# Kernel tuning notes

Measured on AMD Instinct MI355X. Metric: run time of the kernel, lower is better.

## Reference

```python
import jax, jax.numpy as jnp
import numpy as np
import math

NUM_CLASSES = 80
MAX_ANCHOR_MATCHES = 10
ALPHA = 0.5
BETA = 6.0
EPSILON = 1e-9        # label-encoder epsilon
KEPS = 1e-7           # keras.backend.epsilon() used inside compute_ciou
B, NB = 16, 64        # batch, padded max GT boxes


def make_anchor_points():
    # YOLOv8 @ 640x640: strides 8/16/32 -> 80^2 + 40^2 + 20^2 = 8400 anchors
    pts = []
    for stride, n in [(8, 80), (16, 40), (32, 20)]:
        xs = (jnp.arange(n, dtype=jnp.float32) + 0.5) * stride
        gy, gx = jnp.meshgrid(xs, xs, indexing='ij')
        pts.append(jnp.stack([gx.reshape(-1), gy.reshape(-1)], axis=-1))
    return jnp.concatenate(pts, axis=0)  # (8400, 2)


def setup_inputs() -> dict:
    key = jax.random.key(0)
    k0, k1, k2, k3, k4, k5 = jax.random.split(key, 6)
    anc_points = make_anchor_points()
    NA = anc_points.shape[0]
    pd_scores = jax.random.uniform(k0, (B, NA, NUM_CLASSES), dtype=jnp.float32)
    # predicted boxes roughly centered on anchors
    wh = jax.random.uniform(k1, (B, NA, 2), minval=8.0, maxval=96.0)
    ctr = anc_points[None] + jax.random.normal(k2, (B, NA, 2)) * 8.0
    pd_bboxes = jnp.concatenate([ctr - wh / 2, ctr + wh / 2], axis=-1)
    # ground-truth boxes (xyxy) inside a 640x640 image
    g_wh = jax.random.uniform(k3, (B, NB, 2), minval=16.0, maxval=200.0)
    g_ctr = jax.random.uniform(k4, (B, NB, 2), minval=40.0, maxval=600.0)
    gt_bboxes = jnp.concatenate([g_ctr - g_wh / 2, g_ctr + g_wh / 2], axis=-1)
    gt_labels = jax.random.randint(k5, (B, NB), 0, NUM_CLASSES).astype(jnp.float32)
    # first 48 of 64 padded slots are real boxes
    mask_gt = jnp.broadcast_to(jnp.arange(NB)[None, :, None] < 48, (B, NB, 1))
    return {
        'pd_scores': pd_scores,
        'pd_bboxes': pd_bboxes,
        'anc_points': anc_points,
        'gt_labels': gt_labels,
        'gt_bboxes': gt_bboxes,
        'mask_gt': mask_gt,
    }


def compute_ciou(b1, b2):
    """CIoU between xyxy boxes b1 (gt) and b2 (pred); broadcasts, returns (...,)."""
    x1a, y1a, x2a, y2a = b1[..., 0], b1[..., 1], b1[..., 2], b1[..., 3]
    x1b, y1b, x2b, y2b = b2[..., 0], b2[..., 1], b2[..., 2], b2[..., 3]
    w1 = x2a - x1a
    h1 = y2a - y1a + KEPS
    w2 = x2b - x1b
    h2 = y2b - y1b + KEPS
    inter = (jnp.maximum(jnp.minimum(x2a, x2b) - jnp.maximum(x1a, x1b), 0.0)
             * jnp.maximum(jnp.minimum(y2a, y2b) - jnp.maximum(y1a, y1b), 0.0))
    union = w1 * h1 + w2 * h2 - inter + KEPS
    iou = inter / union
    cw = jnp.maximum(x2a, x2b) - jnp.minimum(x1a, x1b)
    ch = jnp.maximum(y2a, y2b) - jnp.minimum(y1a, y1b)
    c2 = cw * cw + ch * ch + KEPS
    rho2 = ((x1a + x2a) / 2 - (x1b + x2b) / 2) ** 2 + ((y1a + y2a) / 2 - (y1b + y2b) / 2) ** 2
    v = (4.0 / math.pi ** 2) * (jnp.arctan(w2 / h2) - jnp.arctan(w1 / h1)) ** 2
    alpha = v / (v - iou + (1.0 + KEPS))
    return iou - (rho2 / c2 + v * alpha)


def _encode(pd_scores, pd_bboxes, anc_points, gt_labels, gt_bboxes, mask_gt):
    Bn, NA, NC = pd_scores.shape
    NBn = gt_bboxes.shape[1]
    f32 = pd_scores.dtype
    mask_gt_b = mask_gt.astype(bool)                      # (B, NB, 1)

    # --- select_candidates_in_gts: anchor center inside gt box ---
    lt = gt_bboxes[:, :, None, :2]                        # (B, NB, 1, 2)
    rb = gt_bboxes[:, :, None, 2:]
    anc = anc_points[None, None, :, :]                    # (1, 1, NA, 2)
    deltas = jnp.concatenate([anc - lt, rb - anc], -1)    # (B, NB, NA, 4)
    mask_in_gts = jnp.min(deltas, axis=-1) > EPSILON      # (B, NB, NA)
    valid = mask_in_gts & mask_gt_b                       # (B, NB, NA)

    # --- get_box_metrics ---
    lbl = jnp.maximum(gt_labels.astype(jnp.int32), 0)     # (B, NB)
    sc = jnp.take_along_axis(pd_scores, jnp.broadcast_to(lbl[:, None, :], (Bn, NA, NBn)), axis=-1)
    sc = jnp.transpose(sc, (0, 2, 1))                     # (B, NB, NA)
    sc = jnp.where(gt_labels[:, :, None] >= 0, sc, 0.0)
    bbox_scores = jnp.where(valid, sc, 0.0)
    iou = compute_ciou(gt_bboxes[:, :, None, :], pd_bboxes[:, None, :, :])  # (B, NB, NA)
    iou = jnp.where(iou > 0, iou, 0.0)
    overlaps = jnp.where(valid, iou, 0.0)
    align_metric = jnp.power(bbox_scores, ALPHA) * jnp.power(overlaps, BETA)

    # --- select_topk_candidates ---
    k = MAX_ANCHOR_MATCHES
    _, topk_idxs = jax.lax.top_k(align_metric, k)         # (B, NB, k)
    topk_idxs = jnp.where(jnp.broadcast_to(mask_gt_b, (Bn, NBn, k)), topk_idxs, 0)
    bi = jnp.arange(Bn)[:, None, None]
    gi = jnp.arange(NBn)[None, :, None]
    counts = jnp.zeros((Bn, NBn, NA), f32).at[bi, gi, topk_idxs].add(1.0)
    mask_topk = jnp.where(counts > 1, 0.0, counts)        # drop idx-0 duplicates
    mask_pos = mask_topk * mask_in_gts.astype(f32) * mask_gt_b.astype(f32)

    # --- select_highest_overlaps (tie-break anchors matched to >1 gt) ---
    fg_mask = jnp.sum(mask_pos, axis=-2)                  # (B, NA)
    mask_multi = jnp.broadcast_to((fg_mask > 1)[:, None, :], (Bn, NBn, NA))
    max_idx = jnp.argmax(overlaps, axis=1)                # (B, NA)
    is_max = jnp.transpose(jax.nn.one_hot(max_idx, NBn, dtype=f32), (0, 2, 1))
    mask_pos = jnp.where(mask_multi, is_max, mask_pos)
    fg_mask = jnp.sum(mask_pos, axis=-2)
    target_gt_idx = jnp.argmax(mask_pos, axis=-2)         # (B, NA)

    # --- get_targets ---
    target_labels = jnp.take_along_axis(lbl, target_gt_idx, axis=1)          # (B, NA)
    target_bboxes = jnp.take_along_axis(gt_bboxes, target_gt_idx[..., None], axis=1)  # (B, NA, 4)
    target_scores = jax.nn.one_hot(target_labels, NC, dtype=f32)
    target_scores = jnp.where((fg_mask > 0)[..., None], target_scores, 0.0)

    # --- normalize class targets by alignment metric ---
    align_metric = align_metric * mask_pos
    pos_align = jnp.max(align_metric, axis=-1, keepdims=True)                # (B, NB, 1)
    pos_overlaps = jnp.max(overlaps * mask_pos, axis=-1, keepdims=True)
    norm = jnp.max(align_metric * pos_overlaps / (pos_align + EPSILON), axis=-2)[..., None]
    target_scores = target_scores * norm
    return target_bboxes, target_scores, fg_mask


def reference(pd_scores, pd_bboxes, anc_points, gt_labels, gt_bboxes, mask_gt):
    tb, ts, fg = _encode(pd_scores, pd_bboxes, anc_points, gt_labels, gt_bboxes, mask_gt)
    return (jax.lax.stop_gradient(tb), jax.lax.stop_gradient(ts), jax.lax.stop_gradient(fg))
```

## Files before the change

### kernel.cpp

```cpp
#include <hip/hip_runtime.h>
#include <cstdint>
#include <cstddef>

#define NBg 64
#define NCg 80
#define KTOP 10
#define K16 16

typedef unsigned long long u64k;

__device__ __forceinline__ float ciou_dev(float gx1, float gy1, float gx2, float gy2,
                                          float px1, float py1, float px2, float py2) {
#pragma clang fp contract(off)
  const float keps = 1e-7f;
  float w1 = gx2 - gx1;
  float h1 = (gy2 - gy1) + keps;
  float w2 = px2 - px1;
  float h2 = (py2 - py1) + keps;
  float iw = fminf(gx2, px2) - fmaxf(gx1, px1);
  float ih = fminf(gy2, py2) - fmaxf(gy1, py1);
  float inter = fmaxf(iw, 0.0f) * fmaxf(ih, 0.0f);
  float uni = w1 * h1 + w2 * h2 - inter + keps;
  float iou = inter / uni;
  float cw = fmaxf(gx2, px2) - fminf(gx1, px1);
  float ch = fmaxf(gy2, py2) - fminf(gy1, py1);
  float c2 = cw * cw + ch * ch + keps;
  float dx = (gx1 + gx2) * 0.5f - (px1 + px2) * 0.5f;
  float dy = (gy1 + gy2) * 0.5f - (py1 + py2) * 0.5f;
  float rho2 = dx * dx + dy * dy;
  float q2 = w2 / h2;
  float q1 = w1 / h1;
  float t = (float)atan((double)q2) - (float)atan((double)q1);
  float v = 0.4052847345693511f * (t * t);
  float alpha = v / ((v - iou) + 1.0000001f);
  return iou - (rho2 / c2 + v * alpha);
}

__device__ __forceinline__ float am_dev(float sc, float ov) {
  float f1 = (float)sqrt((double)sc);
  double o = (double)ov;
  double o3 = o * o * o;
  return f1 * (float)(o3 * o3);
}

__device__ __forceinline__ u64k mk_key(float am, int a) {
  return ((u64k)__float_as_uint(am) << 32) | (unsigned)(~a);
}

__device__ __forceinline__ void merge16(u64k (&L)[K16], const u64k (&B)[K16]) {
  u64k C[K16];
#pragma unroll
  for (int i = 0; i < K16; i++) {
    u64k x = L[i], y = B[15 - i];
    C[i] = x > y ? x : y;
  }
#pragma unroll
  for (int s = 8; s > 0; s >>= 1) {
#pragma unroll
    for (int i = 0; i < K16; i++) {
      if ((i & s) == 0) {
        u64k x = C[i], y = C[i | s];
        C[i] = x > y ? x : y;
        C[i | s] = x > y ? y : x;
      }
    }
  }
#pragma unroll
  for (int i = 0; i < K16; i++) L[i] = C[i];
}

__global__ void ka_topk(const float* __restrict__ pd_scores,
                        const float* __restrict__ pd_bboxes,
                        const float* __restrict__ anc,
                        const float* __restrict__ gt_labels,
                        const float* __restrict__ gt_bboxes,
                        const int* __restrict__ mask_gt,
                        int* __restrict__ sel,
                        float* __restrict__ posAlign,
                        float* __restrict__ posOv,
                        int NA) {
  int row = blockIdx.x;
  int tid = threadIdx.x;
  int lane = tid & 63;
  int wid = tid >> 6;
  if (tid == 0) { posAlign[row] = 0.0f; posOv[row] = 0.0f; }
  if (!mask_gt[row]) {
    if (tid < KTOP) sel[row * KTOP + tid] = -1;
    return;
  }
  int b = row >> 6;
  const float* g = gt_bboxes + (size_t)row * 4;
  float gx1 = g[0], gy1 = g[1], gx2 = g[2], gy2 = g[3];
  float gl = gt_labels[row];
  int lbl = gl > 0.0f ? (int)gl : 0;
  bool glpos = (gl >= 0.0f);

  auto rect = [&](float s, int n, int& x0, int& y0, int& w, int& h) {
    int i0 = (int)floorf(gx1 / s - 0.5f) - 1; if (i0 < 0) i0 = 0;
    int i1 = (int)ceilf (gx2 / s - 0.5f) + 1; if (i1 > n - 1) i1 = n - 1;
    int j0 = (int)floorf(gy1 / s - 0.5f) - 1; if (j0 < 0) j0 = 0;
    int j1 = (int)ceilf (gy2 / s - 0.5f) + 1; if (j1 > n - 1) j1 = n - 1;
    x0 = i0; y0 = j0;
    w = i1 - i0 + 1; h = j1 - j0 + 1;
    if (w < 0) w = 0;
    if (h < 0) h = 0;
  };
  int x00, y00, w0, h0, x01, y01, w1, h1, x02, y02, w2, h2;
  rect( 8.0f, 80, x00, y00, w0, h0);
  rect(16.0f, 40, x01, y01, w1, h1);
  rect(32.0f, 20, x02, y02, w2, h2);
  int sz0 = w0 * h0, sz1 = w1 * h1, sz2 = w2 * h2;
  int tot = sz0 + sz1 + sz2;

  u64k k[KTOP];
#pragma unroll
  for (int q = 0; q < KTOP; q++) k[q] = 0;

  auto ins = [&](u64k key) {
    if (key > k[KTOP - 1]) {
      k[KTOP - 1] = key;
#pragma unroll
      for (int q = KTOP - 1; q > 0; q--) {
        if (k[q] > k[q - 1]) { u64k t = k[q]; k[q] = k[q - 1]; k[q - 1] = t; }
      }
    }
  };

  for (int c = tid; c < tot; c += 256) {
    int cc, x0, y0, w, nbase, ngrid; float ss;
    if (c < sz0)              { cc = c;              x0 = x00; y0 = y00; w = w0; nbase = 0;    ngrid = 80; ss =  8.0f; }
    else if (c < sz0 + sz1)   { cc = c - sz0;        x0 = x01; y0 = y01; w = w1; nbase = 6400; ngrid = 40; ss = 16.0f; }
    else                      { cc = c - sz0 - sz1;  x0 = x02; y0 = y02; w = w2; nbase = 8000; ngrid = 20; ss = 32.0f; }
    int iy = y0 + cc / w;
    int ix = x0 + cc % w;
    float ax = ((float)ix + 0.5f) * ss;
    float ay = ((float)iy + 0.5f) * ss;
    float dmin = fminf(fminf(ax - gx1, ay - gy1), fminf(gx2 - ax, gy2 - ay));
    if (dmin > 1e-9f) {
      int a = nbase + iy * ngrid + ix;
      const float4 pb = ((const float4*)pd_bboxes)[(size_t)b * NA + a];
      float ci = ciou_dev(gx1, gy1, gx2, gy2, pb.x, pb.y, pb.z, pb.w);
      float ov = ci > 0.0f ? ci : 0.0f;
      float sc = glpos ? pd_scores[((size_t)b * NA + a) * NCg + lbl] : 0.0f;
      ins(mk_key(am_dev(sc, ov), a));
    }
  }

  u64k L[K16];
#pragma unroll
  for (int q = 0; q < KTOP; q++) L[q] = k[q];
#pragma unroll
  for (int q = KTOP; q < K16; q++) L[q] = 0;

#pragma unroll
  for (int step = 0; step < 6; step++) {
    u64k B[K16];
#pragma unroll
    for (int q = 0; q < K16; q++)
      B[q] = __shfl_xor((unsigned long long)L[q], 1 << step, 64);
    merge16(L, B);
  }

  __shared__ u64k xl[4][K16];
  if (lane < K16) xl[wid][lane] = L[lane];
  __syncthreads();
  if (wid == 2) {
    u64k B[K16];
#pragma unroll
    for (int q = 0; q < K16; q++) B[q] = xl[3][q];
    merge16(L, B);
    if (lane < K16) xl[2][lane] = L[lane];
  }
  if (wid == 0) {
    u64k B[K16];
#pragma unroll
    for (int q = 0; q < K16; q++) B[q] = xl[1][q];
    merge16(L, B);
  }
  __syncthreads();
  if (wid == 0) {
    u64k B[K16];
#pragma unroll
    for (int q = 0; q < K16; q++) B[q] = xl[2][q];
    merge16(L, B);
    if (lane == 0) {
      int npos = 0;
#pragma unroll
      for (int q = 0; q < KTOP; q++) if ((L[q] >> 32) != 0) npos++;
      int cand = 0;
      const float2* anc2 = (const float2*)anc;
      for (int slot = 0; slot < KTOP; slot++) {
        int a;
        if (slot < npos) {
          a = (int)~(unsigned)L[slot];
        } else {
          bool moved = true;
          while (moved) {
            moved = false;
#pragma unroll
            for (int q = 0; q < KTOP; q++)
              if (q < npos && (int)~(unsigned)L[q] == cand) { cand++; moved = true; }
          }
          a = cand++;
        }
        float2 ap = anc2[a];
        float dmin = fminf(fminf(ap.x - gx1, ap.y - gy1),
                           fminf(gx2 - ap.x, gy2 - ap.y));
        sel[row * KTOP + slot] = (dmin > 1e-9f) ? a : -1;
      }
    }
  }
}

__global__ void k3_resolve(const float* __restrict__ pd_scores,
                           const float* __restrict__ pd_bboxes,
                           const float* __restrict__ anc,
                           const float* __restrict__ gt_labels,
                           const float* __restrict__ gt_bboxes,
                           const int* __restrict__ mask_gt,
                           const int* __restrict__ sel,
                           int* __restrict__ tgt,
                           float* __restrict__ amv,
                           float* __restrict__ out_tb,
                           float* __restrict__ out_fg,
                           float* __restrict__ posAlign,
                           float* __restrict__ posOv,
                           int NA) {
  int b = blockIdx.y;
  int tid = threadIdx.x;
  int a0 = blockIdx.x * 256;
  int a = a0 + tid;
  __shared__ float4 sg[NBg];
  __shared__ int svalid[NBg];
  __shared__ int slbl[NBg];
  __shared__ int sglpos[NBg];
  __shared__ unsigned int mlo[256];
  __shared__ unsigned int mhi[256];
  mlo[tid] = 0u; mhi[tid] = 0u;
  if (tid < NBg) {
    int j = tid;
    const float* g = gt_bboxes + ((size_t)b * NBg + j) * 4;
    sg[j] = make_float4(g[0], g[1], g[2], g[3]);
    svalid[j] = mask_gt[b * NBg + j];
    float gl = gt_labels[b * NBg + j];
    slbl[j] = gl > 0.0f ? (int)gl : 0;
    sglpos[j] = (gl >= 0.0f) ? 1 : 0;
  }
  __syncthreads();
  for (int i = tid; i < NBg * KTOP; i += 256) {
    int e = sel[b * NBg * KTOP + i];
    int d = e - a0;
    if (d >= 0 && d < 256) {
      int j = i / KTOP;
      unsigned int bit = 1u << (j & 31);
      if (j < 32) atomicOr(&mlo[d], bit); else atomicOr(&mhi[d], bit);
    }
  }
  __syncthreads();
  if (a >= NA) return;
  unsigned int lo = mlo[tid], hi = mhi[tid];
  int cnt = __popc(lo) + __popc(hi);
  int first = lo ? (__ffs(lo) - 1) : (hi ? 32 + __ffs(hi) - 1 : 0);

  float ax = anc[2 * a], ay = anc[2 * a + 1];
  float px1 = 0.f, py1 = 0.f, px2 = 0.f, py2 = 0.f;
  if (cnt > 0) {
    const float* pb = pd_bboxes + ((size_t)b * NA + a) * 4;
    px1 = pb[0]; py1 = pb[1]; px2 = pb[2]; py2 = pb[3];
  }
  int t = 0;
  float fg = 0.0f;
  float ovt = -1.0f;
  if (cnt == 1) {
    t = first; fg = 1.0f;
  } else if (cnt > 1) {
    unsigned bm_lo = 0u, bm_hi = 0u;
    for (int jj = 0; jj < NBg; jj++) {
      if (svalid[jj]) {
        float4 gq = sg[jj];
        float dmin = fminf(fminf(ax - gq.x, ay - gq.y), fminf(gq.z - ax, gq.w - ay));
        if (dmin > 1e-9f) {
          if (jj < 32) bm_lo |= 1u << jj; else bm_hi |= 1u << (jj - 32);
        }
      }
    }
    float best = 0.0f;
    t = 0;
    unsigned m = bm_lo; int base = 0;
    for (int half = 0; half < 2; half++) {
      while (m) {
        int jj = base + __ffs(m) - 1; m &= m - 1;
        float4 gq = sg[jj];
        float ci = ciou_dev(gq.x, gq.y, gq.z, gq.w, px1, py1, px2, py2);
        float ov = ci > 0.0f ? ci : 0.0f;
        if (ov > best) { best = ov; t = jj; }
      }
      m = bm_hi; base = 32;
    }
    fg = 1.0f;
    ovt = best;
  }
  tgt[(size_t)b * NA + a] = t;
  out_fg[(size_t)b * NA + a] = fg;
  float4 gb = sg[t];
  ((float4*)out_tb)[(size_t)b * NA + a] = gb;
  float amval = 0.0f;
  if (fg > 0.0f) {
    float ov;
    if (ovt >= 0.0f) {
      ov = ovt;
    } else {
      float ci = ciou_dev(gb.x, gb.y, gb.z, gb.w, px1, py1, px2, py2);
      ov = ci > 0.0f ? ci : 0.0f;
    }
    float sc = sglpos[t] ? pd_scores[((size_t)b * NA + a) * NCg + slbl[t]] : 0.0f;
    amval = am_dev(sc, ov);
    atomicMax((int*)(posAlign + b * NBg + t), __float_as_int(amval));
    atomicMax((int*)(posOv + b * NBg + t), __float_as_int(ov));
  }
  amv[(size_t)b * NA + a] = amval;
}

__global__ void k5_scores(const float* __restrict__ gt_labels,
                          const int* __restrict__ tgt,
                          const float* __restrict__ out_fg,
                          const float* __restrict__ amv,
                          const float* __restrict__ posAlign,
                          const float* __restrict__ posOv,
                          float* __restrict__ out_ts,
                          int NA) {
  int b = blockIdx.y;
  int a0 = blockIdx.x * 256;
  int tid = threadIdx.x;
  int a = a0 + tid;
  __shared__ float snorm[256];
  __shared__ int slab[256];
  float norm = 0.0f;
  int lbl = -1;
  if (a < NA) {
    int t = tgt[(size_t)b * NA + a];
    float fg = out_fg[(size_t)b * NA + a];
    if (fg > 0.0f) {
      float av = amv[(size_t)b * NA + a];
      norm = av * posOv[b * NBg + t] / (posAlign[b * NBg + t] + 1e-9f);
      float gl = gt_labels[b * NBg + t];
      lbl = gl > 0.0f ? (int)gl : 0;
    }
  }
  snorm[tid] = norm;
  slab[tid] = lbl;
  __syncthreads();
  int nanch = NA - a0; if (nanch > 256) nanch = 256;
  int nf4 = nanch * (NCg / 4);
  float4* o = (float4*)(out_ts + ((size_t)b * NA + a0) * NCg);
  for (int i = tid; i < nf4; i += 256) {
    int aa = i / (NCg / 4);
    int c0 = (i % (NCg / 4)) * 4;
    int lb = slab[aa];
    float nv = snorm[aa];
    float4 w = make_float4(0.0f, 0.0f, 0.0f, 0.0f);
    int d = lb - c0;
    if (d >= 0 && d < 4) ((float*)&w)[d] = nv;
    o[i] = w;
  }
}

extern "C" void kernel_launch(void* const* d_in, const int* in_sizes, int n_in,
                              void* d_out, int out_size, void* d_ws, size_t ws_size,
                              hipStream_t stream) {
  const float* pd_scores = (const float*)d_in[0];
  const float* pd_bboxes = (const float*)d_in[1];
  const float* anc       = (const float*)d_in[2];
  const float* gt_labels = (const float*)d_in[3];
  const float* gt_bboxes = (const float*)d_in[4];
  const int*   mask_gt   = (const int*)d_in[5];

  int NA = in_sizes[2] / 2;
  int B  = in_sizes[3] / NBg;
  size_t nBA = (size_t)B * NA;

  float* out_tb = (float*)d_out;
  float* out_ts = out_tb + nBA * 4;
  float* out_fg = out_ts + nBA * NCg;

  char* ws = (char*)d_ws;
  size_t off = 0;
  int* sel = (int*)(ws + off);                off += (size_t)B * NBg * KTOP * 4;
  int* tgt = (int*)(ws + off);                off += nBA * 4;
  float* amv = (float*)(ws + off);            off += nBA * 4;
  float* posAlign = (float*)(ws + off);       off += (size_t)B * NBg * 4;
  float* posOv = (float*)(ws + off);          off += (size_t)B * NBg * 4;

  dim3 blk(256);
  int rows = B * NBg;
  ka_topk<<<rows, blk, 0, stream>>>(pd_scores, pd_bboxes, anc, gt_labels,
                                    gt_bboxes, mask_gt, sel, posAlign, posOv, NA);
  dim3 gA((NA + 255) / 256, B);
  k3_resolve<<<gA, blk, 0, stream>>>(pd_scores, pd_bboxes, anc, gt_labels,
                                     gt_bboxes, mask_gt, sel, tgt, amv,
                                     out_tb, out_fg, posAlign, posOv, NA);
  k5_scores<<<gA, blk, 0, stream>>>(gt_labels, tgt, out_fg, amv, posAlign, posOv,
                                    out_ts, NA);
}
```

Measured before the change: 158.4 us.

## Fuse output zero-fill into top-k kernel and resolve sparsely per batch

The top-k kernel now also writes default values for the dense outputs (target boxes, fg mask and the zeroed score tensor), with each GT-row block covering a slice of anchors. A single per-batch resolve kernel holds the full anchor match bitmask in shared memory, keeps the per-GT max reductions in shared atomics and scatters only the positive anchors into the outputs. This removes the third kernel, the tgt/amv workspace traffic and the global atomics. The cost is that the resolve stage runs only B blocks (16) that each scan 8400 anchors and use about 80KB of shared memory, which means low parallelism.

```diff
diff --git a/kernel.cpp b/kernel.cpp
--- a/kernel.cpp
+++ b/kernel.cpp
@@ -6,6 +6,7 @@
 #define NCg 80
 #define KTOP 10
 #define K16 16
+#define MAXSEL (NBg * KTOP)
 
 typedef unsigned long long u64k;
 
@@ -69,244 +70,252 @@
   for (int i = 0; i < K16; i++) L[i] = C[i];
 }
 
-__global__ void ka_topk(const float* __restrict__ pd_scores,
-                        const float* __restrict__ pd_bboxes,
-                        const float* __restrict__ anc,
-                        const float* __restrict__ gt_labels,
-                        const float* __restrict__ gt_bboxes,
-                        const int* __restrict__ mask_gt,
-                        int* __restrict__ sel,
-                        float* __restrict__ posAlign,
-                        float* __restrict__ posOv,
-                        int NA) {
+__global__ void kac_topk_fill(const float* __restrict__ pd_scores,
+                              const float* __restrict__ pd_bboxes,
+                              const float* __restrict__ anc,
+                              const float* __restrict__ gt_labels,
+                              const float* __restrict__ gt_bboxes,
+                              const int* __restrict__ mask_gt,
+                              int* __restrict__ sel,
+                              float* __restrict__ out_tb,
+                              float* __restrict__ out_ts,
+                              float* __restrict__ out_fg,
+                              int NA) {
   int row = blockIdx.x;
   int tid = threadIdx.x;
   int lane = tid & 63;
   int wid = tid >> 6;
-  if (tid == 0) { posAlign[row] = 0.0f; posOv[row] = 0.0f; }
-  if (!mask_gt[row]) {
+  int b = row >> 6;
+  int j = row & 63;
+  bool rowvalid = mask_gt[row] != 0;
+  const float2* anc2 = (const float2*)anc;
+  __shared__ u64k xl[4][K16];
+
+  if (rowvalid) {
+    const float* g = gt_bboxes + (size_t)row * 4;
+    float gx1 = g[0], gy1 = g[1], gx2 = g[2], gy2 = g[3];
+    float gl = gt_labels[row];
+    int lbl = gl > 0.0f ? (int)gl : 0;
+    bool glpos = (gl >= 0.0f);
+
+    auto rect = [&](float s, int n, int& x0, int& y0, int& w, int& h) {
+      int i0 = (int)floorf(gx1 / s - 0.5f) - 1; if (i0 < 0) i0 = 0;
+      int i1 = (int)ceilf (gx2 / s - 0.5f) + 1; if (i1 > n - 1) i1 = n - 1;
+      int j0 = (int)floorf(gy1 / s - 0.5f) - 1; if (j0 < 0) j0 = 0;
+      int j1 = (int)ceilf (gy2 / s - 0.5f) + 1; if (j1 > n - 1) j1 = n - 1;
+      x0 = i0; y0 = j0;
+      w = i1 - i0 + 1; h = j1 - j0 + 1;
+      if (w < 0) w = 0;
+      if (h < 0) h = 0;
+    };
+    int x00, y00, w0, h0, x01, y01, w1, h1, x02, y02, w2, h2;
+    rect( 8.0f, 80, x00, y00, w0, h0);
+    rect(16.0f, 40, x01, y01, w1, h1);
+    rect(32.0f, 20, x02, y02, w2, h2);
+    int sz0 = w0 * h0, sz1 = w1 * h1, sz2 = w2 * h2;
+    int tot = sz0 + sz1 + sz2;
+
+    u64k k[KTOP];
+#pragma unroll
+    for (int q = 0; q < KTOP; q++) k[q] = 0;
+
+    auto ins = [&](u64k key) {
+      if (key > k[KTOP - 1]) {
+        k[KTOP - 1] = key;
+#pragma unroll
+        for (int q = KTOP - 1; q > 0; q--) {
+          if (k[q] > k[q - 1]) { u64k t = k[q]; k[q] = k[q - 1]; k[q - 1] = t; }
+        }
+      }
+    };
+
+    for (int c = tid; c < tot; c += 256) {
+      int cc, x0, y0, w, nbase, ngrid; float ss;
+      if (c < sz0)            { cc = c;             x0 = x00; y0 = y00; w = w0; nbase = 0;    ngrid = 80; ss =  8.0f; }
+      else if (c < sz0 + sz1) { cc = c - sz0;       x0 = x01; y0 = y01; w = w1; nbase = 6400; ngrid = 40; ss = 16.0f; }
+      else                    { cc = c - sz0 - sz1; x0 = x02; y0 = y02; w = w2; nbase = 8000; ngrid = 20; ss = 32.0f; }
+      int iy = y0 + cc / w;
+      int ix = x0 + cc % w;
+      float ax = ((float)ix + 0.5f) * ss;
+      float ay = ((float)iy + 0.5f) * ss;
+      float dmin = fminf(fminf(ax - gx1, ay - gy1), fminf(gx2 - ax, gy2 - ay));
+      if (dmin > 1e-9f) {
+        int a = nbase + iy * ngrid + ix;
+        const float4 pb = ((const float4*)pd_bboxes)[(size_t)b * NA + a];
+        float ci = ciou_dev(gx1, gy1, gx2, gy2, pb.x, pb.y, pb.z, pb.w);
+        float ov = ci > 0.0f ? ci : 0.0f;
+        float sc = glpos ? pd_scores[((size_t)b * NA + a) * NCg + lbl] : 0.0f;
+        ins(mk_key(am_dev(sc, ov), a));
+      }
+    }
+
+    u64k L[K16];
+#pragma unroll
+    for (int q = 0; q < KTOP; q++) L[q] = k[q];
+#pragma unroll
+    for (int q = KTOP; q < K16; q++) L[q] = 0;
+
+#pragma unroll
+    for (int step = 0; step < 6; step++) {
+      u64k B[K16];
+#pragma unroll
+      for (int q = 0; q < K16; q++)
+        B[q] = __shfl_xor((unsigned long long)L[q], 1 << step, 64);
+      merge16(L, B);
+    }
+    if (lane < K16) xl[wid][lane] = L[lane];
+    __syncthreads();
+    if (wid == 2) {
+      u64k B[K16];
+#pragma unroll
+      for (int q = 0; q < K16; q++) B[q] = xl[3][q];
+      merge16(L, B);
+      if (lane < K16) xl[2][lane] = L[lane];
+    }
+    if (wid == 0) {
+      u64k B[K16];
+#pragma unroll
+      for (int q = 0; q < K16; q++) B[q] = xl[1][q];
+      merge16(L, B);
+    }
+    __syncthreads();
+    if (wid == 0) {
+      u64k B[K16];
+#pragma unroll
+      for (int q = 0; q < K16; q++) B[q] = xl[2][q];
+      merge16(L, B);
+      if (lane == 0) {
+        int npos = 0;
+#pragma unroll
+        for (int q = 0; q < KTOP; q++) if ((L[q] >> 32) != 0) npos++;
+        int cand = 0;
+        for (int slot = 0; slot < KTOP; slot++) {
+          int a;
+          if (slot < npos) {
+            a = (int)~(unsigned)L[slot];
+          } else {
+            bool moved = true;
+            while (moved) {
+              moved = false;
+#pragma unroll
+              for (int q = 0; q < KTOP; q++)
+                if (q < npos && (int)~(unsigned)L[q] == cand) { cand++; moved = true; }
+            }
+            a = cand++;
+          }
+          float2 ap = anc2[a];
+          float dmin = fminf(fminf(ap.x - gx1, ap.y - gy1),
+                             fminf(gx2 - ap.x, gy2 - ap.y));
+          sel[row * KTOP + slot] = (dmin > 1e-9f) ? a : -1;
+        }
+      }
+    }
+  } else {
     if (tid < KTOP) sel[row * KTOP + tid] = -1;
-    return;
-  }
-  int b = row >> 6;
-  const float* g = gt_bboxes + (size_t)row * 4;
-  float gx1 = g[0], gy1 = g[1], gx2 = g[2], gy2 = g[3];
-  float gl = gt_labels[row];
-  int lbl = gl > 0.0f ? (int)gl : 0;
-  bool glpos = (gl >= 0.0f);
-
-  auto rect = [&](float s, int n, int& x0, int& y0, int& w, int& h) {
-    int i0 = (int)floorf(gx1 / s - 0.5f) - 1; if (i0 < 0) i0 = 0;
-    int i1 = (int)ceilf (gx2 / s - 0.5f) + 1; if (i1 > n - 1) i1 = n - 1;
-    int j0 = (int)floorf(gy1 / s - 0.5f) - 1; if (j0 < 0) j0 = 0;
-    int j1 = (int)ceilf (gy2 / s - 0.5f) + 1; if (j1 > n - 1) j1 = n - 1;
-    x0 = i0; y0 = j0;
-    w = i1 - i0 + 1; h = j1 - j0 + 1;
-    if (w < 0) w = 0;
-    if (h < 0) h = 0;
-  };
-  int x00, y00, w0, h0, x01, y01, w1, h1, x02, y02, w2, h2;
-  rect( 8.0f, 80, x00, y00, w0, h0);
-  rect(16.0f, 40, x01, y01, w1, h1);
-  rect(32.0f, 20, x02, y02, w2, h2);
-  int sz0 = w0 * h0, sz1 = w1 * h1, sz2 = w2 * h2;
-  int tot = sz0 + sz1 + sz2;
-
-  u64k k[KTOP];
-#pragma unroll
-  for (int q = 0; q < KTOP; q++) k[q] = 0;
-
-  auto ins = [&](u64k key) {
-    if (key > k[KTOP - 1]) {
-      k[KTOP - 1] = key;
-#pragma unroll
-      for (int q = KTOP - 1; q > 0; q--) {
-        if (k[q] > k[q - 1]) { u64k t = k[q]; k[q] = k[q - 1]; k[q - 1] = t; }
-      }
-    }
-  };
-
-  for (int c = tid; c < tot; c += 256) {
-    int cc, x0, y0, w, nbase, ngrid; float ss;
-    if (c < sz0)              { cc = c;              x0 = x00; y0 = y00; w = w0; nbase = 0;    ngrid = 80; ss =  8.0f; }
-    else if (c < sz0 + sz1)   { cc = c - sz0;        x0 = x01; y0 = y01; w = w1; nbase = 6400; ngrid = 40; ss = 16.0f; }
-    else                      { cc = c - sz0 - sz1;  x0 = x02; y0 = y02; w = w2; nbase = 8000; ngrid = 20; ss = 32.0f; }
-    int iy = y0 + cc / w;
-    int ix = x0 + cc % w;
-    float ax = ((float)ix + 0.5f) * ss;
-    float ay = ((float)iy + 0.5f) * ss;
-    float dmin = fminf(fminf(ax - gx1, ay - gy1), fminf(gx2 - ax, gy2 - ay));
-    if (dmin > 1e-9f) {
-      int a = nbase + iy * ngrid + ix;
-      const float4 pb = ((const float4*)pd_bboxes)[(size_t)b * NA + a];
-      float ci = ciou_dev(gx1, gy1, gx2, gy2, pb.x, pb.y, pb.z, pb.w);
-      float ov = ci > 0.0f ? ci : 0.0f;
-      float sc = glpos ? pd_scores[((size_t)b * NA + a) * NCg + lbl] : 0.0f;
-      ins(mk_key(am_dev(sc, ov), a));
-    }
-  }
-
-  u64k L[K16];
-#pragma unroll
-  for (int q = 0; q < KTOP; q++) L[q] = k[q];
-#pragma unroll
-  for (int q = KTOP; q < K16; q++) L[q] = 0;
-
-#pragma unroll
-  for (int step = 0; step < 6; step++) {
-    u64k B[K16];
-#pragma unroll
-    for (int q = 0; q < K16; q++)
-      B[q] = __shfl_xor((unsigned long long)L[q], 1 << step, 64);
-    merge16(L, B);
-  }
-
-  __shared__ u64k xl[4][K16];
-  if (lane < K16) xl[wid][lane] = L[lane];
-  __syncthreads();
-  if (wid == 2) {
-    u64k B[K16];
-#pragma unroll
-    for (int q = 0; q < K16; q++) B[q] = xl[3][q];
-    merge16(L, B);
-    if (lane < K16) xl[2][lane] = L[lane];
-  }
-  if (wid == 0) {
-    u64k B[K16];
-#pragma unroll
-    for (int q = 0; q < K16; q++) B[q] = xl[1][q];
-    merge16(L, B);
-  }
-  __syncthreads();
-  if (wid == 0) {
-    u64k B[K16];
-#pragma unroll
-    for (int q = 0; q < K16; q++) B[q] = xl[2][q];
-    merge16(L, B);
-    if (lane == 0) {
-      int npos = 0;
-#pragma unroll
-      for (int q = 0; q < KTOP; q++) if ((L[q] >> 32) != 0) npos++;
-      int cand = 0;
-      const float2* anc2 = (const float2*)anc;
-      for (int slot = 0; slot < KTOP; slot++) {
-        int a;
-        if (slot < npos) {
-          a = (int)~(unsigned)L[slot];
-        } else {
-          bool moved = true;
-          while (moved) {
-            moved = false;
-#pragma unroll
-            for (int q = 0; q < KTOP; q++)
-              if (q < npos && (int)~(unsigned)L[q] == cand) { cand++; moved = true; }
-          }
-          a = cand++;
-        }
-        float2 ap = anc2[a];
-        float dmin = fminf(fminf(ap.x - gx1, ap.y - gy1),
-                           fminf(gx2 - ap.x, gy2 - ap.y));
-        sel[row * KTOP + slot] = (dmin > 1e-9f) ? a : -1;
-      }
-    }
-  }
-}
-
-__global__ void k3_resolve(const float* __restrict__ pd_scores,
+  }
+
+  int start = (j * NA) >> 6;
+  int end = ((j + 1) * NA) >> 6;
+  float4 g0 = ((const float4*)gt_bboxes)[(size_t)b * NBg];
+  float4* tb4 = (float4*)out_tb;
+  for (int a = start + tid; a < end; a += 256) {
+    tb4[(size_t)b * NA + a] = g0;
+    out_fg[(size_t)b * NA + a] = 0.0f;
+  }
+  float4 z = make_float4(0.0f, 0.0f, 0.0f, 0.0f);
+  float4* ts4 = (float4*)out_ts + (size_t)b * NA * (NCg / 4);
+  int i0 = start * (NCg / 4), i1 = end * (NCg / 4);
+  for (int i = i0 + tid; i < i1; i += 256) ts4[i] = z;
+}
+
+__global__ void kb_resolve(const float* __restrict__ pd_scores,
                            const float* __restrict__ pd_bboxes,
                            const float* __restrict__ anc,
                            const float* __restrict__ gt_labels,
                            const float* __restrict__ gt_bboxes,
                            const int* __restrict__ mask_gt,
                            const int* __restrict__ sel,
-                           int* __restrict__ tgt,
-                           float* __restrict__ amv,
                            float* __restrict__ out_tb,
+                           float* __restrict__ out_ts,
                            float* __restrict__ out_fg,
-                           float* __restrict__ posAlign,
-                           float* __restrict__ posOv,
                            int NA) {
-  int b = blockIdx.y;
+  int b = blockIdx.x;
   int tid = threadIdx.x;
-  int a0 = blockIdx.x * 256;
-  int a = a0 + tid;
+  __shared__ unsigned mlo[8400], mhi[8400];
   __shared__ float4 sg[NBg];
-  __shared__ int svalid[NBg];
-  __shared__ int slbl[NBg];
-  __shared__ int sglpos[NBg];
-  __shared__ unsigned int mlo[256];
-  __shared__ unsigned int mhi[256];
-  mlo[tid] = 0u; mhi[tid] = 0u;
+  __shared__ int svalid[NBg], slbl[NBg], sglpos[NBg];
+  __shared__ int spaI[NBg], spoI[NBg];
+  __shared__ int ca[MAXSEL], ct[MAXSEL];
+  __shared__ float cam[MAXSEL];
+  __shared__ int scc;
+
+  for (int i = tid; i < 8400; i += 256) { mlo[i] = 0u; mhi[i] = 0u; }
   if (tid < NBg) {
     int j = tid;
-    const float* g = gt_bboxes + ((size_t)b * NBg + j) * 4;
-    sg[j] = make_float4(g[0], g[1], g[2], g[3]);
+    const float* gg = gt_bboxes + ((size_t)b * NBg + j) * 4;
+    sg[j] = make_float4(gg[0], gg[1], gg[2], gg[3]);
     svalid[j] = mask_gt[b * NBg + j];
     float gl = gt_labels[b * NBg + j];
     slbl[j] = gl > 0.0f ? (int)gl : 0;
     sglpos[j] = (gl >= 0.0f) ? 1 : 0;
-  }
+    spaI[j] = 0; spoI[j] = 0;
+  }
+  if (tid == 0) scc = 0;
   __syncthreads();
-  for (int i = tid; i < NBg * KTOP; i += 256) {
-    int e = sel[b * NBg * KTOP + i];
-    int d = e - a0;
-    if (d >= 0 && d < 256) {
+
+  for (int i = tid; i < MAXSEL; i += 256) {
+    int e = sel[b * MAXSEL + i];
+    if (e >= 0) {
       int j = i / KTOP;
-      unsigned int bit = 1u << (j & 31);
-      if (j < 32) atomicOr(&mlo[d], bit); else atomicOr(&mhi[d], bit);
+      if (j < 32) atomicOr(&mlo[e], 1u << j);
+      else        atomicOr(&mhi[e], 1u << (j - 32));
     }
   }
   __syncthreads();
-  if (a >= NA) return;
-  unsigned int lo = mlo[tid], hi = mhi[tid];
-  int cnt = __popc(lo) + __popc(hi);
-  int first = lo ? (__ffs(lo) - 1) : (hi ? 32 + __ffs(hi) - 1 : 0);
-
-  float ax = anc[2 * a], ay = anc[2 * a + 1];
-  float px1 = 0.f, py1 = 0.f, px2 = 0.f, py2 = 0.f;
-  if (cnt > 0) {
+
+  const float2* anc2 = (const float2*)anc;
+  for (int a = tid; a < NA; a += 256) {
+    unsigned lo = mlo[a], hi = mhi[a];
+    if (!(lo | hi)) continue;
+    int cnt = __popc(lo) + __popc(hi);
+    int first = lo ? (__ffs(lo) - 1) : (32 + __ffs(hi) - 1);
     const float* pb = pd_bboxes + ((size_t)b * NA + a) * 4;
-    px1 = pb[0]; py1 = pb[1]; px2 = pb[2]; py2 = pb[3];
-  }
-  int t = 0;
-  float fg = 0.0f;
-  float ovt = -1.0f;
-  if (cnt == 1) {
-    t = first; fg = 1.0f;
-  } else if (cnt > 1) {
-    unsigned bm_lo = 0u, bm_hi = 0u;
-    for (int jj = 0; jj < NBg; jj++) {
-      if (svalid[jj]) {
-        float4 gq = sg[jj];
-        float dmin = fminf(fminf(ax - gq.x, ay - gq.y), fminf(gq.z - ax, gq.w - ay));
-        if (dmin > 1e-9f) {
-          if (jj < 32) bm_lo |= 1u << jj; else bm_hi |= 1u << (jj - 32);
+    float px1 = pb[0], py1 = pb[1], px2 = pb[2], py2 = pb[3];
+    float2 ap = anc2[a];
+    float ax = ap.x, ay = ap.y;
+
+    int t;
+    float ovt = -1.0f;
+    if (cnt == 1) {
+      t = first;
+    } else {
+      unsigned bm_lo = 0u, bm_hi = 0u;
+      for (int jj = 0; jj < NBg; jj++) {
+        if (svalid[jj]) {
+          float4 gq = sg[jj];
+          float dmin = fminf(fminf(ax - gq.x, ay - gq.y), fminf(gq.z - ax, gq.w - ay));
+          if (dmin > 1e-9f) {
+            if (jj < 32) bm_lo |= 1u << jj; else bm_hi |= 1u << (jj - 32);
+          }
         }
       }
-    }
-    float best = 0.0f;
-    t = 0;
-    unsigned m = bm_lo; int base = 0;
-    for (int half = 0; half < 2; half++) {
-      while (m) {
-        int jj = base + __ffs(m) - 1; m &= m - 1;
-        float4 gq = sg[jj];
-        float ci = ciou_dev(gq.x, gq.y, gq.z, gq.w, px1, py1, px2, py2);
-        float ov = ci > 0.0f ? ci : 0.0f;
-        if (ov > best) { best = ov; t = jj; }
-      }
-      m = bm_hi; base = 32;
-    }
-    fg = 1.0f;
-    ovt = best;
-  }
-  tgt[(size_t)b * NA + a] = t;
-  out_fg[(size_t)b * NA + a] = fg;
-  float4 gb = sg[t];
-  ((float4*)out_tb)[(size_t)b * NA + a] = gb;
-  float amval = 0.0f;
-  if (fg > 0.0f) {
+      float best = 0.0f;
+      t = 0;
+      unsigned m = bm_lo; int base = 0;
+      for (int hh = 0; hh < 2; hh++) {
+        while (m) {
+          int jj = base + __ffs(m) - 1; m &= m - 1;
+          float4 gq = sg[jj];
+          float ci = ciou_dev(gq.x, gq.y, gq.z, gq.w, px1, py1, px2, py2);
+          float ov = ci > 0.0f ? ci : 0.0f;
+          if (ov > best) { best = ov; t = jj; }
+        }
+        m = bm_hi; base = 32;
+      }
+      ovt = best;
+    }
     float ov;
+    float4 gb = sg[t];
     if (ovt >= 0.0f) {
       ov = ovt;
     } else {
@@ -314,54 +323,21 @@
       ov = ci > 0.0f ? ci : 0.0f;
     }
     float sc = sglpos[t] ? pd_scores[((size_t)b * NA + a) * NCg + slbl[t]] : 0.0f;
-    amval = am_dev(sc, ov);
-    atomicMax((int*)(posAlign + b * NBg + t), __float_as_int(amval));
-    atomicMax((int*)(posOv + b * NBg + t), __float_as_int(ov));
-  }
-  amv[(size_t)b * NA + a] = amval;
-}
-
-__global__ void k5_scores(const float* __restrict__ gt_labels,
-                          const int* __restrict__ tgt,
-                          const float* __restrict__ out_fg,
-                          const float* __restrict__ amv,
-                          const float* __restrict__ posAlign,
-                          const float* __restrict__ posOv,
-                          float* __restrict__ out_ts,
-                          int NA) {
-  int b = blockIdx.y;
-  int a0 = blockIdx.x * 256;
-  int tid = threadIdx.x;
-  int a = a0 + tid;
-  __shared__ float snorm[256];
-  __shared__ int slab[256];
-  float norm = 0.0f;
-  int lbl = -1;
-  if (a < NA) {
-    int t = tgt[(size_t)b * NA + a];
-    float fg = out_fg[(size_t)b * NA + a];
-    if (fg > 0.0f) {
-      float av = amv[(size_t)b * NA + a];
-      norm = av * posOv[b * NBg + t] / (posAlign[b * NBg + t] + 1e-9f);
-      float gl = gt_labels[b * NBg + t];
-      lbl = gl > 0.0f ? (int)gl : 0;
-    }
-  }
-  snorm[tid] = norm;
-  slab[tid] = lbl;
+    float amval = am_dev(sc, ov);
+    atomicMax(&spaI[t], __float_as_int(amval));
+    atomicMax(&spoI[t], __float_as_int(ov));
+    int p = atomicAdd(&scc, 1);
+    ca[p] = a; ct[p] = t; cam[p] = amval;
+  }
   __syncthreads();
-  int nanch = NA - a0; if (nanch > 256) nanch = 256;
-  int nf4 = nanch * (NCg / 4);
-  float4* o = (float4*)(out_ts + ((size_t)b * NA + a0) * NCg);
-  for (int i = tid; i < nf4; i += 256) {
-    int aa = i / (NCg / 4);
-    int c0 = (i % (NCg / 4)) * 4;
-    int lb = slab[aa];
-    float nv = snorm[aa];
-    float4 w = make_float4(0.0f, 0.0f, 0.0f, 0.0f);
-    int d = lb - c0;
-    if (d >= 0 && d < 4) ((float*)&w)[d] = nv;
-    o[i] = w;
+
+  int n = scc;
+  for (int i = tid; i < n; i += 256) {
+    int a = ca[i], t = ct[i];
+    float norm = cam[i] * __int_as_float(spoI[t]) / (__int_as_float(spaI[t]) + 1e-9f);
+    out_fg[(size_t)b * NA + a] = 1.0f;
+    ((float4*)out_tb)[(size_t)b * NA + a] = sg[t];
+    out_ts[((size_t)b * NA + a) * NCg + slbl[t]] = norm;
   }
 }
 
@@ -383,22 +359,13 @@
   float* out_ts = out_tb + nBA * 4;
   float* out_fg = out_ts + nBA * NCg;
 
-  char* ws = (char*)d_ws;
-  size_t off = 0;
-  int* sel = (int*)(ws + off);                off += (size_t)B * NBg * KTOP * 4;
-  int* tgt = (int*)(ws + off);                off += nBA * 4;
-  float* amv = (float*)(ws + off);            off += nBA * 4;
-  float* posAlign = (float*)(ws + off);       off += (size_t)B * NBg * 4;
-  float* posOv = (float*)(ws + off);          off += (size_t)B * NBg * 4;
+  int* sel = (int*)d_ws;
 
   dim3 blk(256);
-  int rows = B * NBg;
-  ka_topk<<<rows, blk, 0, stream>>>(pd_scores, pd_bboxes, anc, gt_labels,
-                                    gt_bboxes, mask_gt, sel, posAlign, posOv, NA);
-  dim3 gA((NA + 255) / 256, B);
-  k3_resolve<<<gA, blk, 0, stream>>>(pd_scores, pd_bboxes, anc, gt_labels,
-                                     gt_bboxes, mask_gt, sel, tgt, amv,
-                                     out_tb, out_fg, posAlign, posOv, NA);
-  k5_scores<<<gA, blk, 0, stream>>>(gt_labels, tgt, out_fg, amv, posAlign, posOv,
-                                    out_ts, NA);
-}
+  kac_topk_fill<<<B * NBg, blk, 0, stream>>>(pd_scores, pd_bboxes, anc, gt_labels,
+                                             gt_bboxes, mask_gt, sel,
+                                             out_tb, out_ts, out_fg, NA);
+  kb_resolve<<<B, blk, 0, stream>>>(pd_scores, pd_bboxes, anc, gt_labels,
+                                    gt_bboxes, mask_gt, sel,
+                                    out_tb, out_ts, out_fg, NA);
+}
```

Result: slower. 321.4 us (+103.0%).
